# Performance work log

Hardware: AMD Instinct MI355X
Metric: run time of the kernel (lower is better)

The kernel has to match this reference:

```python
import jax, jax.numpy as jnp
import numpy as np
from jax import lax

N_QUBITS = 8
DEPTH = 2
IN_DIM = 512
LN_EPS = 1e-5


def _ry_shared(state, w, theta_w):
    # RY(theta) on wire w, shared angle across the batch. state: [B, 2,...,2]
    ax = w + 1
    c = jnp.cos(theta_w / 2)
    s = jnp.sin(theta_w / 2)
    s0 = lax.index_in_dim(state, 0, axis=ax, keepdims=True)
    s1 = lax.index_in_dim(state, 1, axis=ax, keepdims=True)
    return jnp.concatenate([c * s0 - s * s1, s * s0 + c * s1], axis=ax)


def _cnot(state, cw, tw):
    # CNOT control=cw, target=tw. state: [B, 2,...,2]
    ax_c = cw + 1
    ax_t = tw + 1
    s0 = lax.index_in_dim(state, 0, axis=ax_c, keepdims=True)
    s1 = lax.index_in_dim(state, 1, axis=ax_c, keepdims=True)
    s1 = jnp.flip(s1, axis=ax_t)
    return jnp.concatenate([s0, s1], axis=ax_c)


def _circuit(angles, theta):
    # angles: [B, n]; theta: [n]. Batched statevector sim (RY/CNOT are real).
    B, n = angles.shape
    half = angles * 0.5
    c = jnp.cos(half)
    s = jnp.sin(half)
    # Initial RY layer on |0...0> is a product state: qubit i -> [cos, sin]
    state = jnp.ones((B,), dtype=angles.dtype)
    for i in range(n):
        amp = jnp.stack([c[:, i], s[:, i]], axis=-1)  # [B, 2]
        state = state[..., None] * amp.reshape((B,) + (1,) * i + (2,))
    # state: [B, 2, 2, ..., 2] (n qubit axes)
    for _ in range(DEPTH):
        for i in range(n):
            state = _cnot(state, i, (i + 1) % n)
        for i in range(n):
            state = _ry_shared(state, i, theta[i])
    # <Z_i> = P(bit_i=0) - P(bit_i=1)
    p = state * state
    zs = []
    for i in range(n):
        axes = tuple(a for a in range(1, n + 1) if a != i + 1)
        m = p.sum(axis=axes)  # [B, 2]
        zs.append(m[:, 0] - m[:, 1])
    return jnp.stack(zs, axis=-1)  # [B, n]


def setup_inputs() -> dict:
    key = jax.random.key(0)
    ks = jax.random.split(key, 6)
    B = 131072
    return {
        "E": jax.random.normal(ks[0], (B, IN_DIM), dtype=jnp.float32),
        "ln_gamma": jnp.ones((IN_DIM,), dtype=jnp.float32),
        "ln_beta": jnp.zeros((IN_DIM,), dtype=jnp.float32),
        "W_pre": jax.random.normal(ks[1], (N_QUBITS, IN_DIM), dtype=jnp.float32) * (1.0 / np.sqrt(IN_DIM)),
        "b_pre": jax.random.normal(ks[2], (N_QUBITS,), dtype=jnp.float32) * 0.02,
        "theta": jax.random.normal(ks[3], (N_QUBITS,), dtype=jnp.float32) * 0.1,
        "W_post": jax.random.normal(ks[4], (1, N_QUBITS), dtype=jnp.float32) * (1.0 / np.sqrt(N_QUBITS)),
        "b_post": jax.random.normal(ks[5], (1,), dtype=jnp.float32) * 0.02,
    }


def reference(E, ln_gamma, ln_beta, W_pre, b_pre, theta, W_post, b_post):
    # pre: LayerNorm + Linear(in_dim -> n_qubits)
    mu = E.mean(axis=-1, keepdims=True)
    var = ((E - mu) ** 2).mean(axis=-1, keepdims=True)
    x = (E - mu) * lax.rsqrt(var + LN_EPS) * ln_gamma + ln_beta
    angles = x @ W_pre.T + b_pre  # [B, n_qubits]
    Z = _circuit(angles, theta)  # [B, n_qubits]
    logit_known = (Z @ W_post.T + b_post)[:, 0]  # squeeze(-1)
    return logit_known
```

## Files before the change

kernel.cpp:

```cpp
#include <hip/hip_runtime.h>

#define BLOCK 256

__device__ __forceinline__ float rfl(float x) {
  return __uint_as_float(__builtin_amdgcn_readfirstlane(__float_as_uint(x)));
}

template<int CTRL>
__device__ __forceinline__ float dppmov(float x) {
  return __int_as_float(__builtin_amdgcn_update_dpp(
      0, __float_as_int(x), CTRL, 0xf, 0xf, true));
}
__device__ __forceinline__ float dx1(float x) { return dppmov<0xB1>(x); }
__device__ __forceinline__ float dx2(float x) { return dppmov<0x4E>(x); }
__device__ __forceinline__ float dx4(float x) {
  return dppmov<0x1B>(dppmov<0x141>(x));
}
__device__ __forceinline__ float dx8(float x) { return dppmov<0x128>(x); }
__device__ __forceinline__ float sx16(float x) { return __shfl_xor(x, 16, 64); }
__device__ __forceinline__ float sx32(float x) { return __shfl_xor(x, 32, 64); }

__device__ __forceinline__ float wave_allsum(float x) {
  x += dx1(x); x += dx2(x); x += dx4(x); x += dx8(x);
  x += sx16(x); x += sx32(x);
  return x;
}


__global__ __launch_bounds__(BLOCK, 4) void qsco_kernel(
    const float* __restrict__ E,
    const float* __restrict__ ln_gamma,
    const float* __restrict__ ln_beta,
    const float* __restrict__ Wpre,
    const float* __restrict__ bpre,
    const float* __restrict__ theta,
    const float* __restrict__ Wpost,
    const float* __restrict__ bpost,
    float* __restrict__ out,
    int nrows)
{
  __shared__ float Wg[8][512];

  const int tid  = threadIdx.x;
  const int lane = tid & 63;

#pragma unroll
  for (int t = 0; t < 4; ++t) {
    const int e4 = (t * BLOCK + tid) << 2;
    const int j = e4 >> 9, k = e4 & 511;
    const float4 w = *(const float4*)(Wpre + j * 512 + k);
    const float4 g = *(const float4*)(ln_gamma + k);
    float4 r;
    r.x = w.x * g.x; r.y = w.y * g.y; r.z = w.z * g.z; r.w = w.w * g.w;
    *(float4*)(&Wg[j][k]) = r;
  }
  __syncthreads();

  const int k0 = lane << 3;
  const float4 gamA = *(const float4*)(ln_gamma + k0);
  const float4 gamB = *(const float4*)(ln_gamma + k0 + 4);
  const float4 betA = *(const float4*)(ln_beta + k0);
  const float4 betB = *(const float4*)(ln_beta + k0 + 4);
  float G[8], K[8];
#pragma unroll
  for (int j = 0; j < 8; ++j) {
    const float4 wA = *(const float4*)(Wpre + j * 512 + k0);
    const float4 wB = *(const float4*)(Wpre + j * 512 + k0 + 4);
    const float gs = wA.x*gamA.x + wA.y*gamA.y + wA.z*gamA.z + wA.w*gamA.w
                   + wB.x*gamB.x + wB.y*gamB.y + wB.z*gamB.z + wB.w*gamB.w;
    const float ks = wA.x*betA.x + wA.y*betA.y + wA.z*betA.z + wA.w*betA.w
                   + wB.x*betB.x + wB.y*betB.y + wB.z*betB.z + wB.w*betB.w;
    G[j] = rfl(wave_allsum(gs));
    K[j] = rfl(wave_allsum(ks) + bpre[j]);
  }

  float cT[8], sT[8];
#pragma unroll
  for (int q = 0; q < 8; ++q) {
    const float h = 0.5f * theta[q];
    cT[q] = rfl(__cosf(h));
    sT[q] = rfl(__sinf(h));
  }
  const float ss6 = (lane & 1) ? sT[6] : -sT[6];
  const float ss7 = (lane & 2) ? sT[7] : -sT[7];

  float al[8];
#pragma unroll
  for (int q = 0; q < 8; ++q) al[q] = rfl(Wpost[q]);
  const float lsign = ((lane & 1) ? -al[6] : al[6]) + ((lane & 2) ? -al[7] : al[7]);
  const float bp = rfl(bpost[0]);

  const int wave = blockIdx.x * (BLOCK / 64) + (tid >> 6);
  const int row  = wave * 16 + (lane >> 2);
  const int sub  = lane & 3;
  const float* Erow = E + (size_t)(row < nrows ? row : 0) * 512 + (sub << 2);

  float f[10];
#pragma unroll
  for (int t = 0; t < 10; ++t) f[t] = 0.f;
#pragma unroll 4
  for (int i = 0; i < 32; ++i) {
    const float4 ev = *(const float4*)(Erow + (i << 4));
    const int kk = (sub << 2) + (i << 4);
    f[0] += (ev.x + ev.y) + (ev.z + ev.w);
    f[1] += ev.x*ev.x + ev.y*ev.y + ev.z*ev.z + ev.w*ev.w;
#pragma unroll
    for (int j = 0; j < 8; ++j) {
      const float4 w = *(const float4*)(&Wg[j][kk]);
      f[2 + j] += ev.x*w.x + ev.y*w.y + ev.z*w.z + ev.w*w.w;
    }
  }
#pragma unroll
  for (int t = 0; t < 10; ++t) f[t] += dx1(f[t]);
#pragma unroll
  for (int t = 0; t < 10; ++t) f[t] += dx2(f[t]);

  const float mu   = f[0] * (1.0f / 512.0f);
  const float var  = f[1] * (1.0f / 512.0f) - mu * mu;
  const float rstd = rsqrtf(var + 1e-5f);

  float ca[8], sa[8];
#pragma unroll
  for (int j = 0; j < 8; ++j) {
    const float ang = rstd * (f[2 + j] - mu * G[j]) + K[j];
    const float h = 0.5f * ang;
    ca[j] = __cosf(h);
    sa[j] = __sinf(h);
  }

  float a[64];
  a[0] = ((lane & 1) ? sa[6] : ca[6]) * ((lane & 2) ? sa[7] : ca[7]);
#pragma unroll
  for (int b = 0; b < 6; ++b) {
    const int m = 1 << b;
#pragma unroll
    for (int k = 0; k < 32; ++k) {
      if (k < m) {
        a[k + m] = a[k] * sa[b];
        a[k]     = a[k] * ca[b];
      }
    }
  }

#pragma unroll
  for (int d = 0; d < 2; ++d) {
#pragma unroll
    for (int k = 0; k < 64; ++k) if ((k & 1) && !(k & 2)) {
      const float t_ = a[k]; a[k] = a[k ^ 2]; a[k ^ 2] = t_;
    }
#pragma unroll
    for (int k = 0; k < 64; ++k) if ((k & 2) && !(k & 4)) {
      const float t_ = a[k]; a[k] = a[k ^ 4]; a[k ^ 4] = t_;
    }
#pragma unroll
    for (int k = 0; k < 64; ++k) if ((k & 4) && !(k & 8)) {
      const float t_ = a[k]; a[k] = a[k ^ 8]; a[k ^ 8] = t_;
    }
#pragma unroll
    for (int k = 0; k < 64; ++k) if ((k & 8) && !(k & 16)) {
      const float t_ = a[k]; a[k] = a[k ^ 16]; a[k ^ 16] = t_;
    }
#pragma unroll
    for (int k = 0; k < 64; ++k) if ((k & 16) && !(k & 32)) {
      const float t_ = a[k]; a[k] = a[k ^ 32]; a[k ^ 32] = t_;
    }
#pragma unroll
    for (int k = 32; k < 64; ++k) a[k] = dx1(a[k]);
    {
      const bool c = (lane & 1) != 0;
#pragma unroll
      for (int k = 0; k < 64; ++k) {
        const float t_ = dx2(a[k]);
        a[k] = c ? t_ : a[k];
      }
    }
    {
      const bool c = (lane & 2) != 0;
#pragma unroll
      for (int m = 0; m < 32; ++m) {
        const float x = a[2 * m], y = a[2 * m + 1];
        a[2 * m]     = c ? y : x;
        a[2 * m + 1] = c ? x : y;
      }
    }
#pragma unroll
    for (int i = 0; i < 6; ++i) {
      const int m = 1 << i;
      const float cc = cT[i], sn = sT[i];
#pragma unroll
      for (int k = 0; k < 64; ++k) if (!(k & m)) {
        const float x = a[k], y = a[k | m];
        a[k]     = cc * x - sn * y;
        a[k | m] = sn * x + cc * y;
      }
    }
#pragma unroll
    for (int k = 0; k < 64; ++k) {
      const float p = dx1(a[k]);
      a[k] = cT[6] * a[k] + ss6 * p;
    }
#pragma unroll
    for (int k = 0; k < 64; ++k) {
      const float p = dx2(a[k]);
      a[k] = cT[7] * a[k] + ss7 * p;
    }
  }

#pragma unroll
  for (int k = 0; k < 64; ++k) a[k] = a[k] * a[k];
  float zr[6];
#pragma unroll
  for (int b = 0; b < 6; ++b) {
    const int n = 32 >> b;
    float zb = 0.f;
#pragma unroll
    for (int m = 0; m < 32; ++m) {
      if (m < n) {
        const float p = a[2 * m], q = a[2 * m + 1];
        zb   += (p - q);
        a[m]  = p + q;
      }
    }
    zr[b] = zb;
  }
  float vL = lsign * a[0];
#pragma unroll
  for (int i = 0; i < 6; ++i) vL += al[i] * zr[i];
  vL += dx1(vL);
  vL += dx2(vL);
  if (sub == 0 && row < nrows) out[row] = vL + bp;
}

extern "C" void kernel_launch(void* const* d_in, const int* in_sizes, int n_in,
                              void* d_out, int out_size, void* d_ws, size_t ws_size,
                              hipStream_t stream) {
  const float* E        = (const float*)d_in[0];
  const float* ln_gamma = (const float*)d_in[1];
  const float* ln_beta  = (const float*)d_in[2];
  const float* Wpre     = (const float*)d_in[3];
  const float* bpre     = (const float*)d_in[4];
  const float* theta    = (const float*)d_in[5];
  const float* Wpost    = (const float*)d_in[6];
  const float* bpost    = (const float*)d_in[7];
  float* out = (float*)d_out;

  const int nrows = in_sizes[0] / 512;
  const int rows_per_block = (BLOCK / 64) * 16;
  const int grid = (nrows + rows_per_block - 1) / rows_per_block;
  qsco_kernel<<<grid, BLOCK, 0, stream>>>(E, ln_gamma, ln_beta, Wpre, bpre,
                                          theta, Wpost, bpost, out, nrows);
}
```

Baseline: 405.5 us.

## Use packed FP32 math for LN projection and statevector simulation

Repacks the 64-amplitude per-lane statevector into 32 float2 vectors, with qubit 5 as the packed pair, and the dot-product accumulators into float2 form so the compiler can emit v_pk_fma_f32 / v_pk_mul_f32 packed instructions. CNOTs that cross the pair boundary are reworked into a swap inside each pair, a DPP move on one half, and a new DPP lane permutation (0x6C). This is meant to roughly halve VALU instruction count in the compute-heavy circuit and projection stages. Costs include extra element shuffles between halves, per-half DPP moves, and possible register-pairing constraints that could hurt occupancy.

After: 392.4 us. -3.2%, faster.

```diff
diff --git a/kernel.cpp b/kernel.cpp
--- a/kernel.cpp
+++ b/kernel.cpp
@@ -1,10 +1,18 @@
 #include <hip/hip_runtime.h>
 
 #define BLOCK 256
+
+typedef float v2f __attribute__((ext_vector_type(2)));
 
 __device__ __forceinline__ float rfl(float x) {
   return __uint_as_float(__builtin_amdgcn_readfirstlane(__float_as_uint(x)));
 }
+__device__ __forceinline__ v2f mk2(float x, float y) { v2f r; r.x = x; r.y = y; return r; }
+__device__ __forceinline__ v2f sp2(float x) { v2f r; r.x = x; r.y = x; return r; }
+__device__ __forceinline__ v2f pkfma(v2f a, v2f b, v2f c) {
+  return __builtin_elementwise_fma(a, b, c);
+}
+__device__ __forceinline__ v2f swap2(v2f v) { return __builtin_shufflevector(v, v, 1, 0); }
 
 template<int CTRL>
 __device__ __forceinline__ float dppmov(float x) {
@@ -13,6 +21,7 @@
 }
 __device__ __forceinline__ float dx1(float x) { return dppmov<0xB1>(x); }
 __device__ __forceinline__ float dx2(float x) { return dppmov<0x4E>(x); }
+__device__ __forceinline__ float dswap13(float x) { return dppmov<0x6C>(x); }
 __device__ __forceinline__ float dx4(float x) {
   return dppmov<0x1B>(dppmov<0x141>(x));
 }
@@ -95,21 +104,25 @@
   const int sub  = lane & 3;
   const float* Erow = E + (size_t)(row < nrows ? row : 0) * 512 + (sub << 2);
 
-  float f[10];
-#pragma unroll
-  for (int t = 0; t < 10; ++t) f[t] = 0.f;
+  v2f f2[10];
+#pragma unroll
+  for (int t = 0; t < 10; ++t) f2[t] = sp2(0.f);
 #pragma unroll 4
   for (int i = 0; i < 32; ++i) {
     const float4 ev = *(const float4*)(Erow + (i << 4));
+    const v2f eA = mk2(ev.x, ev.y), eB = mk2(ev.z, ev.w);
     const int kk = (sub << 2) + (i << 4);
-    f[0] += (ev.x + ev.y) + (ev.z + ev.w);
-    f[1] += ev.x*ev.x + ev.y*ev.y + ev.z*ev.z + ev.w*ev.w;
+    f2[0] += eA + eB;
+    f2[1] = pkfma(eA, eA, pkfma(eB, eB, f2[1]));
 #pragma unroll
     for (int j = 0; j < 8; ++j) {
       const float4 w = *(const float4*)(&Wg[j][kk]);
-      f[2 + j] += ev.x*w.x + ev.y*w.y + ev.z*w.z + ev.w*w.w;
-    }
-  }
+      f2[2 + j] = pkfma(eA, mk2(w.x, w.y), pkfma(eB, mk2(w.z, w.w), f2[2 + j]));
+    }
+  }
+  float f[10];
+#pragma unroll
+  for (int t = 0; t < 10; ++t) f[t] = f2[t].x + f2[t].y;
 #pragma unroll
   for (int t = 0; t < 10; ++t) f[t] += dx1(f[t]);
 #pragma unroll
@@ -128,104 +141,125 @@
     sa[j] = __sinf(h);
   }
 
-  float a[64];
-  a[0] = ((lane & 1) ? sa[6] : ca[6]) * ((lane & 2) ? sa[7] : ca[7]);
-#pragma unroll
-  for (int b = 0; b < 6; ++b) {
-    const int m = 1 << b;
-#pragma unroll
-    for (int k = 0; k < 32; ++k) {
-      if (k < m) {
-        a[k + m] = a[k] * sa[b];
-        a[k]     = a[k] * ca[b];
+  v2f a2[32];
+  {
+    const float base = ((lane & 1) ? sa[6] : ca[6]) * ((lane & 2) ? sa[7] : ca[7]);
+    a2[0] = mk2(ca[5] * base, sa[5] * base);
+#pragma unroll
+    for (int b = 0; b < 5; ++b) {
+      const int m = 1 << b;
+      const v2f cb = sp2(ca[b]), sb = sp2(sa[b]);
+#pragma unroll
+      for (int k = 0; k < 16; ++k) {
+        if (k < m) {
+          a2[k + m] = a2[k] * sb;
+          a2[k]     = a2[k] * cb;
+        }
       }
     }
   }
 
+  const v2f cT2_0 = sp2(cT[0]), sT2_0 = sp2(sT[0]), nT2_0 = sp2(-sT[0]);
+  const v2f cT2_1 = sp2(cT[1]), sT2_1 = sp2(sT[1]), nT2_1 = sp2(-sT[1]);
+  const v2f cT2_2 = sp2(cT[2]), sT2_2 = sp2(sT[2]), nT2_2 = sp2(-sT[2]);
+  const v2f cT2_3 = sp2(cT[3]), sT2_3 = sp2(sT[3]), nT2_3 = sp2(-sT[3]);
+  const v2f cT2_4 = sp2(cT[4]), sT2_4 = sp2(sT[4]), nT2_4 = sp2(-sT[4]);
+  const v2f cT2_5 = sp2(cT[5]);
+  const v2f sm5   = mk2(-sT[5], sT[5]);
+  const v2f cT2_6 = sp2(cT[6]), ss6v = sp2(ss6);
+  const v2f cT2_7 = sp2(cT[7]), ss7v = sp2(ss7);
+
+#define RY_REG(CC, SS, NN, M) { \
+    _Pragma("unroll") \
+    for (int k = 0; k < 32; ++k) if (!(k & (M))) { \
+      const v2f x = a2[k], y = a2[k | (M)]; \
+      a2[k]       = pkfma(NN, y, CC * x); \
+      a2[k | (M)] = pkfma(SS, x, CC * y); \
+    } }
+
 #pragma unroll
   for (int d = 0; d < 2; ++d) {
 #pragma unroll
-    for (int k = 0; k < 64; ++k) if ((k & 1) && !(k & 2)) {
-      const float t_ = a[k]; a[k] = a[k ^ 2]; a[k ^ 2] = t_;
-    }
-#pragma unroll
-    for (int k = 0; k < 64; ++k) if ((k & 2) && !(k & 4)) {
-      const float t_ = a[k]; a[k] = a[k ^ 4]; a[k ^ 4] = t_;
-    }
-#pragma unroll
-    for (int k = 0; k < 64; ++k) if ((k & 4) && !(k & 8)) {
-      const float t_ = a[k]; a[k] = a[k ^ 8]; a[k ^ 8] = t_;
-    }
-#pragma unroll
-    for (int k = 0; k < 64; ++k) if ((k & 8) && !(k & 16)) {
-      const float t_ = a[k]; a[k] = a[k ^ 16]; a[k ^ 16] = t_;
-    }
-#pragma unroll
-    for (int k = 0; k < 64; ++k) if ((k & 16) && !(k & 32)) {
-      const float t_ = a[k]; a[k] = a[k ^ 32]; a[k ^ 32] = t_;
-    }
-#pragma unroll
-    for (int k = 32; k < 64; ++k) a[k] = dx1(a[k]);
-    {
-      const bool c = (lane & 1) != 0;
-#pragma unroll
-      for (int k = 0; k < 64; ++k) {
-        const float t_ = dx2(a[k]);
-        a[k] = c ? t_ : a[k];
-      }
+    for (int k = 0; k < 32; ++k) if ((k & 1) && !(k & 2)) {
+      const v2f t_ = a2[k]; a2[k] = a2[k ^ 2]; a2[k ^ 2] = t_;
+    }
+#pragma unroll
+    for (int k = 0; k < 32; ++k) if ((k & 2) && !(k & 4)) {
+      const v2f t_ = a2[k]; a2[k] = a2[k ^ 4]; a2[k ^ 4] = t_;
+    }
+#pragma unroll
+    for (int k = 0; k < 32; ++k) if ((k & 4) && !(k & 8)) {
+      const v2f t_ = a2[k]; a2[k] = a2[k ^ 8]; a2[k ^ 8] = t_;
+    }
+#pragma unroll
+    for (int k = 0; k < 32; ++k) if ((k & 8) && !(k & 16)) {
+      const v2f t_ = a2[k]; a2[k] = a2[k ^ 16]; a2[k ^ 16] = t_;
+    }
+#pragma unroll
+    for (int k = 16; k < 32; ++k) a2[k] = swap2(a2[k]);
+#pragma unroll
+    for (int k = 0; k < 32; ++k) a2[k].y = dx1(a2[k].y);
+#pragma unroll
+    for (int k = 0; k < 32; ++k) {
+      a2[k].x = dswap13(a2[k].x);
+      a2[k].y = dswap13(a2[k].y);
     }
     {
       const bool c = (lane & 2) != 0;
 #pragma unroll
-      for (int m = 0; m < 32; ++m) {
-        const float x = a[2 * m], y = a[2 * m + 1];
-        a[2 * m]     = c ? y : x;
-        a[2 * m + 1] = c ? x : y;
+      for (int m = 0; m < 16; ++m) {
+        const v2f x = a2[2 * m], y = a2[2 * m + 1];
+        a2[2 * m].x     = c ? y.x : x.x;
+        a2[2 * m].y     = c ? y.y : x.y;
+        a2[2 * m + 1].x = c ? x.x : y.x;
+        a2[2 * m + 1].y = c ? x.y : y.y;
       }
     }
-#pragma unroll
-    for (int i = 0; i < 6; ++i) {
-      const int m = 1 << i;
-      const float cc = cT[i], sn = sT[i];
-#pragma unroll
-      for (int k = 0; k < 64; ++k) if (!(k & m)) {
-        const float x = a[k], y = a[k | m];
-        a[k]     = cc * x - sn * y;
-        a[k | m] = sn * x + cc * y;
+    RY_REG(cT2_0, sT2_0, nT2_0, 1)
+    RY_REG(cT2_1, sT2_1, nT2_1, 2)
+    RY_REG(cT2_2, sT2_2, nT2_2, 4)
+    RY_REG(cT2_3, sT2_3, nT2_3, 8)
+    RY_REG(cT2_4, sT2_4, nT2_4, 16)
+#pragma unroll
+    for (int k = 0; k < 32; ++k) {
+      const v2f t_ = swap2(a2[k]);
+      a2[k] = pkfma(sm5, t_, cT2_5 * a2[k]);
+    }
+#pragma unroll
+    for (int k = 0; k < 32; ++k) {
+      const v2f p = mk2(dx1(a2[k].x), dx1(a2[k].y));
+      a2[k] = pkfma(ss6v, p, cT2_6 * a2[k]);
+    }
+#pragma unroll
+    for (int k = 0; k < 32; ++k) {
+      const v2f p = mk2(dx2(a2[k].x), dx2(a2[k].y));
+      a2[k] = pkfma(ss7v, p, cT2_7 * a2[k]);
+    }
+  }
+#undef RY_REG
+
+#pragma unroll
+  for (int k = 0; k < 32; ++k) a2[k] = a2[k] * a2[k];
+  v2f zr2[5];
+#pragma unroll
+  for (int b = 0; b < 5; ++b) {
+    const int n = 16 >> b;
+    v2f zb = sp2(0.f);
+#pragma unroll
+    for (int m = 0; m < 16; ++m) {
+      if (m < n) {
+        const v2f p = a2[2 * m], q = a2[2 * m + 1];
+        zb   += (p - q);
+        a2[m] = p + q;
       }
     }
-#pragma unroll
-    for (int k = 0; k < 64; ++k) {
-      const float p = dx1(a[k]);
-      a[k] = cT[6] * a[k] + ss6 * p;
-    }
-#pragma unroll
-    for (int k = 0; k < 64; ++k) {
-      const float p = dx2(a[k]);
-      a[k] = cT[7] * a[k] + ss7 * p;
-    }
-  }
-
-#pragma unroll
-  for (int k = 0; k < 64; ++k) a[k] = a[k] * a[k];
-  float zr[6];
-#pragma unroll
-  for (int b = 0; b < 6; ++b) {
-    const int n = 32 >> b;
-    float zb = 0.f;
-#pragma unroll
-    for (int m = 0; m < 32; ++m) {
-      if (m < n) {
-        const float p = a[2 * m], q = a[2 * m + 1];
-        zb   += (p - q);
-        a[m]  = p + q;
-      }
-    }
-    zr[b] = zb;
-  }
-  float vL = lsign * a[0];
-#pragma unroll
-  for (int i = 0; i < 6; ++i) vL += al[i] * zr[i];
+    zr2[b] = zb;
+  }
+  const float z5  = a2[0].x - a2[0].y;
+  const float tot = a2[0].x + a2[0].y;
+  float vL = lsign * tot + al[5] * z5;
+#pragma unroll
+  for (int b = 0; b < 5; ++b) vL += al[b] * (zr2[b].x + zr2[b].y);
   vL += dx1(vL);
   vL += dx2(vL);
   if (sub == 0 && row < nrows) out[row] = vL + bp;
```
